# Kernel tuning notes

Measured on AMD Instinct MI355X. Metric: run time of the kernel, lower is better.

## Reference

```python
import jax, jax.numpy as jnp
from jax import lax
import numpy as np

B, W, V, E, H = 512, 40, 12000, 512, 512


def setup_inputs() -> dict:
    key = jax.random.key(0)
    ks = jax.random.split(key, 9)
    s = 0.05
    ques_vec = jax.random.randint(ks[0], (B, W), 0, V + 1)          # token ids, 0 = pad
    ques_len = jax.random.randint(ks[1], (B,), 1, W + 1)             # valid lengths in [1, W]
    lookup_W = jax.random.normal(ks[2], (E, V), jnp.float32) * s     # nn.Linear(vocab, emb).weight
    wih0 = jax.random.normal(ks[3], (2, 4 * H, E), jnp.float32) * s  # [dir, 4H, in]
    whh0 = jax.random.normal(ks[4], (2, 4 * H, H), jnp.float32) * s
    b0 = jax.random.normal(ks[5], (2, 2, 4 * H), jnp.float32) * s    # [dir, {b_ih,b_hh}, 4H]
    wih1 = jax.random.normal(ks[6], (2, 4 * H, 2 * H), jnp.float32) * s
    whh1 = jax.random.normal(ks[7], (2, 4 * H, H), jnp.float32) * s
    b1 = jax.random.normal(ks[8], (2, 2, 4 * H), jnp.float32) * s
    return {"ques_vec": ques_vec, "ques_len": ques_len, "lookup_W": lookup_W,
            "wih0": wih0, "whh0": whh0, "b0": b0,
            "wih1": wih1, "whh1": whh1, "b1": b1}


def _lstm_dir(x, wih, whh, b, reverse):
    # x: [B, T, D]; PyTorch gate order i, f, g, o
    Hc = whh.shape[1]
    xg = jnp.einsum('btd,gd->btg', x, wih) + b[0] + b[1]  # [B, T, 4H]
    xs = jnp.swapaxes(xg, 0, 1)                            # [T, B, 4H]
    if reverse:
        xs = xs[::-1]

    def step(carry, g_t):
        h, c = carry
        g = g_t + h @ whh.T
        i, f, gg, o = jnp.split(g, 4, axis=-1)
        c = jax.nn.sigmoid(f) * c + jax.nn.sigmoid(i) * jnp.tanh(gg)
        h = jax.nn.sigmoid(o) * jnp.tanh(c)
        return (h, c), h

    h0 = jnp.zeros((x.shape[0], Hc), x.dtype)
    _, hs = lax.scan(step, (h0, h0), xs)
    if reverse:
        hs = hs[::-1]
    return jnp.swapaxes(hs, 0, 1)  # [B, T, H]


def _bilstm(x, wih, whh, b):
    fwd = _lstm_dir(x, wih[0], whh[0], b[0], False)
    bwd = _lstm_dir(x, wih[1], whh[1], b[1], True)
    return jnp.concatenate([fwd, bwd], axis=-1)  # [B, T, 2H]


def reference(ques_vec, ques_len, lookup_W, wih0, whh0, b0, wih1, whh1, b1):
    # one-hot over vocab+1 with column 0 dropped == gather with id 0 -> zero vector
    table = jnp.concatenate([jnp.zeros((1, E), lookup_W.dtype), lookup_W.T], axis=0)  # [V+1, E]
    emb = jnp.tanh(table[ques_vec])          # [B, W, E] (dropout=0 -> identity)
    h = _bilstm(emb, wih0, whh0, b0)         # layer 0
    h = _bilstm(h, wih1, whh1, b1)           # layer 1 -> [B, W, 2H]
    # scatter-mask bmm == select hidden state at timestep ques_len-1
    idx = (ques_len - 1)[:, None, None]
    return jnp.take_along_axis(h, idx, axis=1).reshape(ques_vec.shape[0], -1)  # [B, 2H]
```

## Files before the change

### kernel.cpp

```cpp
#include <hip/hip_runtime.h>
#include <hip/hip_bf16.h>
#include <stdint.h>

#define NB 512
#define NW 40
#define NE 512
#define NH 512
#define NV 12000
#define G4 2048

typedef unsigned short u16;
typedef unsigned int u32;
typedef unsigned long long u64;
typedef __attribute__((ext_vector_type(8))) short short8;
typedef __attribute__((ext_vector_type(4))) float f32x4;

__device__ __forceinline__ unsigned short f2bf(float f) {
  unsigned int u = __float_as_uint(f);
  u += 0x7FFF + ((u >> 16) & 1);
  return (unsigned short)(u >> 16);
}
__device__ __forceinline__ float bf2f(unsigned short b) {
  return __uint_as_float(((unsigned int)b) << 16);
}
__device__ __forceinline__ float loadIn(const void* p, long i, int bf) {
  return bf ? bf2f(((const u16*)p)[i]) : ((const float*)p)[i];
}
__device__ __forceinline__ float fast_tanh(float x) {
  float ax = __builtin_fabsf(x);
  float t = 1.f - 2.f * __builtin_amdgcn_rcpf(__expf(ax + ax) + 1.f);
  return __builtin_copysignf(t, x);
}
__device__ __forceinline__ float sigm(float x) {
  return __builtin_amdgcn_rcpf(1.f + __expf(-x));
}

__global__ void detect_kernel(const u16* p, int* flag) {
  __shared__ int cnt;
  int i = threadIdx.x;
  if (i == 0) cnt = 0;
  __syncthreads();
  unsigned short u = p[2 * (i * 1001)];
  int e = (u >> 7) & 0xFF;
  if (e >= 100 && e <= 126) atomicAdd(&cnt, 1);
  __syncthreads();
  if (i == 0) *flag = (cnt >= 32) ? 1 : 0;
}

__global__ void table_kernel(const void* lookup, const int* flag, u16* tableT) {
  __shared__ float tile[64][65];
  int bf = *flag;
  int v0 = blockIdx.x * 64, e0 = blockIdx.y * 64;
  int tx = threadIdx.x, ty = threadIdx.y;
#pragma unroll
  for (int r = 0; r < 16; ++r) {
    int e = r * 4 + ty, v = tx;
    if (v0 + v < NV)
      tile[e][v] = tanhf(loadIn(lookup, (long)(e0 + e) * NV + v0 + v, bf));
  }
  __syncthreads();
#pragma unroll
  for (int r = 0; r < 16; ++r) {
    int v = r * 4 + ty, e = tx;
    if (v0 + v < NV)
      tableT[(long)(v0 + v) * NE + e0 + e] = f2bf(tile[e][v]);
  }
}

__global__ void embed_kernel(const int* __restrict__ qv,
                             const u16* __restrict__ tableT,
                             u16* __restrict__ emb) {
  int tid = blockIdx.x * 256 + threadIdx.x;
  int token = tid >> 6;
  int chunk = tid & 63;
  int tt = token / NB, b = token % NB;
  int q = qv[b * NW + tt];
  uint4 val = make_uint4(0u, 0u, 0u, 0u);
  if (q > 0) val = *(const uint4*)(tableT + (long)(q - 1) * NE + chunk * 8);
  *(uint4*)(emb + (long)token * NE + chunk * 8) = val;
}

__global__ void pack_kernel(const void* wih0, const void* whh0, const void* b0,
                            const void* wih1, const void* whh1, const void* b1,
                            const int* flag, u16* Wc0, u16* Wc1, float* bsum) {
  const long N0 = 2L * G4 * 1024, N1 = 2L * G4 * 1536;
  long idx = (long)blockIdx.x * 256 + threadIdx.x;
  int bf = *flag;
  if (idx < N0) {
    int d = (int)(idx / (G4 * 1024));
    int rem = (int)(idx % (long)(G4 * 1024));
    int g = rem / 1024, k = rem % 1024;
    float v = (k < 512) ? loadIn(wih0, ((long)d * G4 + g) * 512 + k, bf)
                        : loadIn(whh0, ((long)d * G4 + g) * 512 + (k - 512), bf);
    Wc0[idx] = f2bf(v);
  } else if (idx < N0 + N1) {
    long i2 = idx - N0;
    int d = (int)(i2 / (G4 * 1536));
    int rem = (int)(i2 % (long)(G4 * 1536));
    int g = rem / 1536, k = rem % 1536;
    float v = (k < 1024) ? loadIn(wih1, ((long)d * G4 + g) * 1024 + k, bf)
                         : loadIn(whh1, ((long)d * G4 + g) * 512 + (k - 1024), bf);
    Wc1[i2] = f2bf(v);
  } else if (idx < N0 + N1 + 2L * 2 * G4) {
    long i3 = idx - N0 - N1;
    int layer = (int)(i3 / (2 * G4));
    int d = (int)((i3 / G4) & 1);
    int g = (int)(i3 % G4);
    const void* bb = layer ? b1 : b0;
    float v = loadIn(bb, (long)d * 2 * G4 + g, bf) +
              loadIn(bb, (long)d * 2 * G4 + G4 + g, bf);
    bsum[i3] = v;
  }
}

__global__ void zero_bar(unsigned int* bar) {
  bar[blockIdx.x * 256 + threadIdx.x] = 0u;
}

__global__ __launch_bounds__(256, 2) void xg_gemm(
    const u16* __restrict__ X, int Kx, int Kfull, const u16* __restrict__ Wc,
    const float* __restrict__ bsumL, u16* __restrict__ xg) {
  __shared__ __align__(16) char lds[32768];
  const int tid = threadIdx.x;
  const int lane = tid & 63, wv = tid >> 6;
  const int wm = wv & 1, wn = wv >> 1;
  const int col = lane & 15, quad = lane >> 4;
  const int s = blockIdx.x >> 5, w = blockIdx.x & 31;
  const int bx = (s % 40) * 4 + (w & 3);
  const int by = (s / 40) * 8 + (w >> 2);
  const int tb0 = bx * 128;
  const int d = by >> 4, colb = by & 15, j0 = colb * 32;

  f32x4 zero = {0.f, 0.f, 0.f, 0.f};
  f32x4 acc[4][4];
#pragma unroll
  for (int i = 0; i < 4; ++i)
#pragma unroll
    for (int j = 0; j < 4; ++j) acc[i][j] = zero;

  const int iters = Kx >> 6;
  for (int it = 0; it < iters; ++it) {
    int k0 = it << 6;
#pragma unroll
    for (int p = 0; p < 8; ++p) {
      int c = p * 256 + tid;
      const u16* gsrc;
      if (c < 1024) {
        int r = c >> 3, sl = c & 7;
        int kk = k0 + ((sl * 8) ^ ((r & 7) << 3));
        gsrc = X + (long)(tb0 + r) * Kx + kk;
      } else {
        int cb = c - 1024;
        int r = cb >> 3, sl = cb & 7;
        int kk = k0 + ((sl * 8) ^ ((r & 7) << 3));
        int grow = (r >> 5) * 512 + j0 + (r & 31);
        gsrc = Wc + ((long)d * G4 + grow) * Kfull + kk;
      }
      __builtin_amdgcn_global_load_lds(
          (const __attribute__((address_space(1))) void*)(const void*)gsrc,
          (__attribute__((address_space(3))) void*)(lds + p * 4096 + wv * 1024),
          16, 0, 0);
    }
    __syncthreads();
    const u16* As = (const u16*)lds;
    const u16* Bs = (const u16*)(lds + 16384);
#pragma unroll
    for (int ks = 0; ks < 2; ++ks) {
      short8 afr[4], bfr[4];
#pragma unroll
      for (int mf = 0; mf < 4; ++mf) {
        int rm = wm * 64 + mf * 16 + col;
        int sl = (ks * 32 + quad * 8) ^ ((rm & 7) << 3);
        afr[mf] = *(const short8*)(As + rm * 64 + sl);
      }
#pragma unroll
      for (int nf = 0; nf < 4; ++nf) {
        int br = wn * 64 + nf * 16 + col;
        int sl = (ks * 32 + quad * 8) ^ ((br & 7) << 3);
        bfr[nf] = *(const short8*)(Bs + br * 64 + sl);
      }
#pragma unroll
      for (int mf = 0; mf < 4; ++mf)
#pragma unroll
        for (int nf = 0; nf < 4; ++nf)
          acc[mf][nf] = __builtin_amdgcn_mfma_f32_16x16x32_bf16(
              afr[mf], bfr[nf], acc[mf][nf], 0, 0, 0);
    }
    __syncthreads();
  }

  float bias[4];
#pragma unroll
  for (int nf = 0; nf < 4; ++nf) {
    int n = wn * 64 + nf * 16 + col;
    bias[nf] = bsumL[d * G4 + (n >> 5) * 512 + j0 + (n & 31)];
  }
#pragma unroll
  for (int mf = 0; mf < 4; ++mf)
#pragma unroll
    for (int nf = 0; nf < 4; ++nf) {
      int n = wn * 64 + nf * 16 + col;
      int g = n >> 5, jn = n & 31;
#pragma unroll
      for (int r = 0; r < 4; ++r) {
        int m = wm * 64 + mf * 16 + quad * 4 + r;
        int tb = tb0 + m, t = tb >> 9, b = tb & 511;
        long oi = ((((long)t * 2 + d) * 16 + colb) * 512 + b) * 128 + jn * 4 + g;
        xg[oi] = f2bf(acc[mf][nf][r] + bias[nf]);
      }
    }
}

__global__ __launch_bounds__(256, 1) void lstm_pers(
    const u16* __restrict__ xg, const u16* __restrict__ Wc, int Kfull, int Kx,
    u16* __restrict__ hbuf, u16* __restrict__ h0cat, void* __restrict__ outp,
    const int* __restrict__ qlen, const int* __restrict__ flag,
    unsigned int* bar, int layer) {
  __shared__ __align__(16) char lds[163840];
  const int tid = threadIdx.x;
  const int lane = tid & 63, wv = tid >> 6;
  const int col = lane & 15, quad = lane >> 4;
  const int l = blockIdx.x;
  const int colid = l & 31, mi = l >> 5;
  const int colb = colid & 15, d = colid >> 4;
  const int j0 = colb * 32;
  const int m0 = mi * 64;
  const int gid = l >> 4;
  const int r0 = wv * 16;

#pragma unroll
  for (int p = 0; p < 32; ++p) {
    int c = p * 256 + tid;
    int row = c >> 6, rem = c & 63;
    int kc = rem >> 3, sl = rem & 7;
    int grow = (row >> 5) * 512 + j0 + (row & 31);
    int gk = Kx + kc * 64 + ((sl * 8) ^ ((row & 7) << 3));
    const u16* gsrc = Wc + ((long)d * G4 + grow) * Kfull + gk;
    __builtin_amdgcn_global_load_lds(
        (const __attribute__((address_space(1))) void*)(const void*)gsrc,
        (__attribute__((address_space(3))) void*)(lds + p * 4096 + wv * 1024),
        16, 0, 0);
  }
  const u16* Bs = (const u16*)lds;
  char* wbuf = lds + 131072 + wv * 8192;
  u16* packb = (u16*)wbuf;

  float creg[2][4];
#pragma unroll
  for (int i = 0; i < 2; ++i)
#pragma unroll
    for (int r = 0; r < 4; ++r) creg[i][r] = 0.f;
  const int isbf = *flag;
  f32x4 zero = {0.f, 0.f, 0.f, 0.f};

  __syncthreads();

#pragma unroll 1
  for (int t = 0; t < NW; ++t) {
    const int tq = d ? (NW - 1 - t) : t;

    ushort4 xgv[2][4];
    const u16* xgt =
        xg + ((((long)tq * 2 + d) * 16 + colb) * 512 + m0 + r0) * 128;
#pragma unroll
    for (int js = 0; js < 2; ++js)
#pragma unroll
      for (int r = 0; r < 4; ++r)
        xgv[js][r] =
            *(const ushort4*)(xgt + (quad * 4 + r) * 128 + (js * 16 + col) * 4);
    __builtin_amdgcn_sched_barrier(0);

    f32x4 acc[8];
#pragma unroll
    for (int g = 0; g < 8; ++g) acc[g] = zero;

    if (t > 0) {
      {
        u32* sp = bar + ((gid * 4 + wv) << 4) + col;
        while (__ballot((int)(__hip_atomic_load(sp, __ATOMIC_RELAXED,
                                                __HIP_MEMORY_SCOPE_AGENT) <
                              (u32)t)))
          __builtin_amdgcn_s_sleep(1);
      }
      __builtin_amdgcn_sched_barrier(0);

      const u16* hp = hbuf + ((t - 1) & 1) * (2L * NB * NH) +
                      ((long)d * NB + m0 + r0) * NH;
      auto stage = [&](int it) {
        char* dst = wbuf + (it & 1) * 4096;
#pragma unroll
        for (int i = 0; i < 4; ++i) {
          int c = i * 64 + lane;
          int row = c >> 4, slot = c & 15;
          int half = slot >> 3, ck = slot & 7;
          int kk = it * 128 + half * 64 + ((ck * 8) ^ ((row & 7) << 3));
          const u16* gsrc = hp + (long)row * NH + kk;
          __builtin_amdgcn_global_load_lds(
              (const __attribute__((address_space(1))) void*)(const void*)gsrc,
              (__attribute__((address_space(3))) void*)(dst + i * 1024), 16, 0,
              16 );
        }
      };
      stage(0);
      stage(1);
#pragma unroll
      for (int it = 0; it < 4; ++it) {
        if (it < 3)
          asm volatile("s_waitcnt vmcnt(4)" ::: "memory");
        else
          asm volatile("s_waitcnt vmcnt(0)" ::: "memory");
        const u16* As = (const u16*)(wbuf + (it & 1) * 4096);
        short8 afr[4];
#pragma unroll
        for (int ks = 0; ks < 4; ++ks) {
          int ksub = ks * 32 + quad * 8;
          afr[ks] = *(const short8*)(As + col * 128 + (ksub & 64) +
                                     ((ksub & 63) ^ ((col & 7) << 3)));
        }
        if (it < 2) {
          asm volatile("s_waitcnt lgkmcnt(0)" ::: "memory");
          __builtin_amdgcn_sched_barrier(0);
          stage(it + 2);
        }
#pragma unroll
        for (int ks = 0; ks < 4; ++ks) {
          const int kc = it * 128 + ks * 32 + quad * 8;
#pragma unroll
          for (int nf = 0; nf < 8; ++nf) {
            int br = nf * 16 + col;
            int slb = (kc & 63) ^ ((br & 7) << 3);
            short8 bfr = *(const short8*)(Bs + br * 512 + (kc & ~63) + slb);
            acc[nf] = __builtin_amdgcn_mfma_f32_16x16x32_bf16(afr[ks], bfr,
                                                              acc[nf], 0, 0, 0);
          }
        }
      }
    }

#pragma unroll
    for (int js = 0; js < 2; ++js)
#pragma unroll
      for (int r = 0; r < 4; ++r) {
        const u16* xv = (const u16*)&xgv[js][r];
        float gi = acc[0 * 2 + js][r] + bf2f(xv[0]);
        float gf = acc[1 * 2 + js][r] + bf2f(xv[1]);
        float gg = acc[2 * 2 + js][r] + bf2f(xv[2]);
        float go = acc[3 * 2 + js][r] + bf2f(xv[3]);
        float si = sigm(gi);
        float sf = sigm(gf);
        float so = sigm(go);
        float cn = sf * creg[js][r] + si * fast_tanh(gg);
        float h = so * fast_tanh(cn);
        creg[js][r] = cn;
        packb[(quad * 4 + r) * 32 + js * 16 + col] = f2bf(h);
        if (layer == 1 && !isbf) {
          int bg = m0 + r0 + quad * 4 + r;
          if (qlen[bg] - 1 == tq)
            ((float*)outp)[(long)bg * (2 * NH) + d * NH + j0 + js * 16 + col] =
                h;
        }
      }

    const int srow = lane >> 2, part = lane & 3;
    u64 v0, v1;
    {
      const u64* pp = (const u64*)(packb + srow * 32 + part * 8);
      v0 = pp[0];
      v1 = pp[1];
    }
    u16* hnxt = hbuf + (t & 1) * (2L * NB * NH);
    {
      u64* hdst = (u64*)(hnxt + ((long)d * NB + m0 + r0 + srow) * NH + j0 +
                         part * 8);
      __hip_atomic_store(hdst, v0, __ATOMIC_RELAXED, __HIP_MEMORY_SCOPE_AGENT);
      __hip_atomic_store(hdst + 1, v1, __ATOMIC_RELAXED,
                         __HIP_MEMORY_SCOPE_AGENT);
    }

    if (t < NW - 1) {
      asm volatile("s_waitcnt vmcnt(0)" ::: "memory");
      if (lane == 0)
        __hip_atomic_store(bar + ((gid * 4 + wv) << 4) + colb, (u32)(t + 1),
                           __ATOMIC_RELAXED, __HIP_MEMORY_SCOPE_AGENT);
    }

    if (layer == 0) {
      u16* dst = h0cat + ((long)tq * NB + m0 + r0 + srow) * (2 * NH) + d * NH +
                 j0 + part * 8;
      *(u64*)dst = v0;
      *((u64*)dst + 1) = v1;
    } else if (isbf) {
      int bg = m0 + r0 + srow;
      if (qlen[bg] - 1 == tq) {
        u16* dst = (u16*)outp + (long)bg * (2 * NH) + d * NH + j0 + part * 8;
        *(u64*)dst = v0;
        *((u64*)dst + 1) = v1;
      }
    }
    __builtin_amdgcn_sched_barrier(0);
  }
}

extern "C" void kernel_launch(void* const* d_in, const int* in_sizes, int n_in,
                              void* d_out, int out_size, void* d_ws,
                              size_t ws_size, hipStream_t stream) {
  const int* qv = (const int*)d_in[0];
  const int* ql = (const int*)d_in[1];
  const void* lookup = d_in[2];
  const void* wih0 = d_in[3];
  const void* whh0 = d_in[4];
  const void* b0 = d_in[5];
  const void* wih1 = d_in[6];
  const void* whh1 = d_in[7];
  const void* b1 = d_in[8];

  char* ws = (char*)d_ws;
  size_t off = 0;
  int* flag = (int*)ws;                 off += 256;
  unsigned int* bar = (unsigned int*)(ws + off); off += 8192;
  float* bsum = (float*)(ws + off);     off += 2L * 2 * G4 * 4;
  u16* Wc0 = (u16*)(ws + off);          off += 2L * G4 * 1024 * 2;
  u16* Wc1 = (u16*)(ws + off);          off += 2L * G4 * 1536 * 2;
  u16* hbuf = (u16*)(ws + off);         off += 2L * 2 * NB * NH * 2;
  u16* h0cat = (u16*)(ws + off);        off += (size_t)NW * NB * 2 * NH * 2;
  u16* emb = (u16*)(ws + off);          off += (size_t)NW * NB * NE * 2;
  u16* xg = (u16*)(ws + off);           off += (size_t)NW * 2 * 16 * 512 * 128 * 2;
  u16* tableT = h0cat;

  detect_kernel<<<1, 64, 0, stream>>>((const u16*)lookup, flag);
  table_kernel<<<dim3(188, 8), dim3(64, 4), 0, stream>>>(lookup, flag, tableT);
  {
    long total = 2L * G4 * 1024 + 2L * G4 * 1536 + 2L * 2 * G4;
    int blocks = (int)((total + 255) / 256);
    pack_kernel<<<blocks, 256, 0, stream>>>(wih0, whh0, b0, wih1, whh1, b1,
                                            flag, Wc0, Wc1, bsum);
  }
  embed_kernel<<<NW * NB / 4, 256, 0, stream>>>(qv, tableT, emb);

  xg_gemm<<<5120, 256, 0, stream>>>(emb, 512, 1024, Wc0, bsum, xg);
  zero_bar<<<8, 256, 0, stream>>>(bar);
  lstm_pers<<<256, 256, 0, stream>>>(xg, Wc0, 1024, 512, hbuf, h0cat, d_out,
                                     ql, flag, bar, 0);
  xg_gemm<<<5120, 256, 0, stream>>>(h0cat, 1024, 1536, Wc1, bsum + 2 * G4, xg);
  zero_bar<<<8, 256, 0, stream>>>(bar);
  lstm_pers<<<256, 256, 0, stream>>>(xg, Wc1, 1536, 1024, hbuf, h0cat, d_out,
                                     ql, flag, bar, 1);
}
```

Measured before the change: 1.002 ms.

## Split persistent LSTM across 512 blocks with half-width column tiles

The persistent recurrent kernel now uses 512 blocks, each owning 16 hidden columns instead of 32. This halves the per-block LDS footprint so two blocks can be resident per CU, and spreads the serial per-timestep h@Whh work across more CUs. The layer-0 hidden output is written in a column-tiled layout, and the layer-1 input GEMM reads that layout through a new xtiled flag. The cost is more barrier flags to poll per step and smaller, less efficient MFMA tiles per wave.

```diff
diff --git a/kernel.cpp b/kernel.cpp
--- a/kernel.cpp
+++ b/kernel.cpp
@@ -118,8 +118,9 @@
 }
 
 __global__ __launch_bounds__(256, 2) void xg_gemm(
-    const u16* __restrict__ X, int Kx, int Kfull, const u16* __restrict__ Wc,
-    const float* __restrict__ bsumL, u16* __restrict__ xg) {
+    const u16* __restrict__ X, int Kx, int Kfull, int xtiled,
+    const u16* __restrict__ Wc, const float* __restrict__ bsumL,
+    u16* __restrict__ xg) {
   __shared__ __align__(16) char lds[32768];
   const int tid = threadIdx.x;
   const int lane = tid & 63, wv = tid >> 6;
@@ -148,7 +149,13 @@
       if (c < 1024) {
         int r = c >> 3, sl = c & 7;
         int kk = k0 + ((sl * 8) ^ ((r & 7) << 3));
-        gsrc = X + (long)(tb0 + r) * Kx + kk;
+        int tb = tb0 + r;
+        if (xtiled) {
+          gsrc = X + ((long)(tb >> 9) * 64 + (kk >> 4)) * 8192 +
+                 (long)(tb & 511) * 16 + (kk & 15);
+        } else {
+          gsrc = X + (long)tb * Kx + kk;
+        }
       } else {
         int cb = c - 1024;
         int r = cb >> 3, sl = cb & 7;
@@ -211,29 +218,29 @@
     }
 }
 
-__global__ __launch_bounds__(256, 1) void lstm_pers(
+__global__ __launch_bounds__(256, 2) void lstm_pers(
     const u16* __restrict__ xg, const u16* __restrict__ Wc, int Kfull, int Kx,
     u16* __restrict__ hbuf, u16* __restrict__ h0cat, void* __restrict__ outp,
     const int* __restrict__ qlen, const int* __restrict__ flag,
     unsigned int* bar, int layer) {
-  __shared__ __align__(16) char lds[163840];
+  __shared__ __align__(16) char lds[81920];
   const int tid = threadIdx.x;
   const int lane = tid & 63, wv = tid >> 6;
   const int col = lane & 15, quad = lane >> 4;
   const int l = blockIdx.x;
-  const int colid = l & 31, mi = l >> 5;
-  const int colb = colid & 15, d = colid >> 4;
-  const int j0 = colb * 32;
+  const int cb = l & 31;
+  const int gid = l >> 5;
+  const int d = gid & 1, mi = gid >> 1;
+  const int j0 = cb * 16;
   const int m0 = mi * 64;
-  const int gid = l >> 4;
   const int r0 = wv * 16;
 
 #pragma unroll
-  for (int p = 0; p < 32; ++p) {
+  for (int p = 0; p < 16; ++p) {
     int c = p * 256 + tid;
     int row = c >> 6, rem = c & 63;
     int kc = rem >> 3, sl = rem & 7;
-    int grow = (row >> 5) * 512 + j0 + (row & 31);
+    int grow = (row >> 4) * 512 + j0 + (row & 15);
     int gk = Kx + kc * 64 + ((sl * 8) ^ ((row & 7) << 3));
     const u16* gsrc = Wc + ((long)d * G4 + grow) * Kfull + gk;
     __builtin_amdgcn_global_load_lds(
@@ -242,14 +249,12 @@
         16, 0, 0);
   }
   const u16* Bs = (const u16*)lds;
-  char* wbuf = lds + 131072 + wv * 8192;
+  char* wbuf = lds + 65536 + wv * 4096;
   u16* packb = (u16*)wbuf;
 
-  float creg[2][4];
-#pragma unroll
-  for (int i = 0; i < 2; ++i)
-#pragma unroll
-    for (int r = 0; r < 4; ++r) creg[i][r] = 0.f;
+  float creg[4];
+#pragma unroll
+  for (int r = 0; r < 4; ++r) creg[r] = 0.f;
   const int isbf = *flag;
   f32x4 zero = {0.f, 0.f, 0.f, 0.f};
 
@@ -259,24 +264,22 @@
   for (int t = 0; t < NW; ++t) {
     const int tq = d ? (NW - 1 - t) : t;
 
-    ushort4 xgv[2][4];
+    ushort4 xgv[4];
     const u16* xgt =
-        xg + ((((long)tq * 2 + d) * 16 + colb) * 512 + m0 + r0) * 128;
-#pragma unroll
-    for (int js = 0; js < 2; ++js)
-#pragma unroll
-      for (int r = 0; r < 4; ++r)
-        xgv[js][r] =
-            *(const ushort4*)(xgt + (quad * 4 + r) * 128 + (js * 16 + col) * 4);
+        xg + ((((long)tq * 2 + d) * 16 + (cb >> 1)) * 512 + m0 + r0) * 128;
+#pragma unroll
+    for (int r = 0; r < 4; ++r)
+      xgv[r] =
+          *(const ushort4*)(xgt + (quad * 4 + r) * 128 + ((cb & 1) * 16 + col) * 4);
     __builtin_amdgcn_sched_barrier(0);
 
-    f32x4 acc[8];
-#pragma unroll
-    for (int g = 0; g < 8; ++g) acc[g] = zero;
+    f32x4 acc[4];
+#pragma unroll
+    for (int g = 0; g < 4; ++g) acc[g] = zero;
 
     if (t > 0) {
       {
-        u32* sp = bar + ((gid * 4 + wv) << 4) + col;
+        u32* sp = bar + ((gid * 4 + wv) << 5) + (lane & 31);
         while (__ballot((int)(__hip_atomic_load(sp, __ATOMIC_RELAXED,
                                                 __HIP_MEMORY_SCOPE_AGENT) <
                               (u32)t)))
@@ -287,13 +290,12 @@
       const u16* hp = hbuf + ((t - 1) & 1) * (2L * NB * NH) +
                       ((long)d * NB + m0 + r0) * NH;
       auto stage = [&](int it) {
-        char* dst = wbuf + (it & 1) * 4096;
-#pragma unroll
-        for (int i = 0; i < 4; ++i) {
+        char* dst = wbuf + (it & 1) * 2048;
+#pragma unroll
+        for (int i = 0; i < 2; ++i) {
           int c = i * 64 + lane;
-          int row = c >> 4, slot = c & 15;
-          int half = slot >> 3, ck = slot & 7;
-          int kk = it * 128 + half * 64 + ((ck * 8) ^ ((row & 7) << 3));
+          int row = c >> 3, slot = c & 7;
+          int kk = it * 64 + ((slot * 8) ^ ((row & 7) << 3));
           const u16* gsrc = hp + (long)row * NH + kk;
           __builtin_amdgcn_global_load_lds(
               (const __attribute__((address_space(1))) void*)(const void*)gsrc,
@@ -303,30 +305,29 @@
       };
       stage(0);
       stage(1);
-#pragma unroll
-      for (int it = 0; it < 4; ++it) {
-        if (it < 3)
-          asm volatile("s_waitcnt vmcnt(4)" ::: "memory");
+#pragma unroll 1
+      for (int it = 0; it < 8; ++it) {
+        if (it < 7)
+          asm volatile("s_waitcnt vmcnt(2)" ::: "memory");
         else
           asm volatile("s_waitcnt vmcnt(0)" ::: "memory");
-        const u16* As = (const u16*)(wbuf + (it & 1) * 4096);
-        short8 afr[4];
-#pragma unroll
-        for (int ks = 0; ks < 4; ++ks) {
+        const u16* As = (const u16*)(wbuf + (it & 1) * 2048);
+        short8 afr[2];
+#pragma unroll
+        for (int ks = 0; ks < 2; ++ks) {
           int ksub = ks * 32 + quad * 8;
-          afr[ks] = *(const short8*)(As + col * 128 + (ksub & 64) +
-                                     ((ksub & 63) ^ ((col & 7) << 3)));
+          afr[ks] = *(const short8*)(As + col * 64 + (ksub ^ ((col & 7) << 3)));
         }
-        if (it < 2) {
+        if (it < 6) {
           asm volatile("s_waitcnt lgkmcnt(0)" ::: "memory");
           __builtin_amdgcn_sched_barrier(0);
           stage(it + 2);
         }
 #pragma unroll
-        for (int ks = 0; ks < 4; ++ks) {
-          const int kc = it * 128 + ks * 32 + quad * 8;
-#pragma unroll
-          for (int nf = 0; nf < 8; ++nf) {
+        for (int ks = 0; ks < 2; ++ks) {
+          const int kc = it * 64 + ks * 32 + quad * 8;
+#pragma unroll
+          for (int nf = 0; nf < 4; ++nf) {
             int br = nf * 16 + col;
             int slb = (kc & 63) ^ ((br & 7) << 3);
             short8 bfr = *(const short8*)(Bs + br * 512 + (kc & ~63) + slb);
@@ -338,63 +339,49 @@
     }
 
 #pragma unroll
-    for (int js = 0; js < 2; ++js)
-#pragma unroll
-      for (int r = 0; r < 4; ++r) {
-        const u16* xv = (const u16*)&xgv[js][r];
-        float gi = acc[0 * 2 + js][r] + bf2f(xv[0]);
-        float gf = acc[1 * 2 + js][r] + bf2f(xv[1]);
-        float gg = acc[2 * 2 + js][r] + bf2f(xv[2]);
-        float go = acc[3 * 2 + js][r] + bf2f(xv[3]);
-        float si = sigm(gi);
-        float sf = sigm(gf);
-        float so = sigm(go);
-        float cn = sf * creg[js][r] + si * fast_tanh(gg);
-        float h = so * fast_tanh(cn);
-        creg[js][r] = cn;
-        packb[(quad * 4 + r) * 32 + js * 16 + col] = f2bf(h);
-        if (layer == 1 && !isbf) {
-          int bg = m0 + r0 + quad * 4 + r;
-          if (qlen[bg] - 1 == tq)
-            ((float*)outp)[(long)bg * (2 * NH) + d * NH + j0 + js * 16 + col] =
-                h;
-        }
-      }
+    for (int r = 0; r < 4; ++r) {
+      const u16* xv = (const u16*)&xgv[r];
+      float gi = acc[0][r] + bf2f(xv[0]);
+      float gf = acc[1][r] + bf2f(xv[1]);
+      float gg = acc[2][r] + bf2f(xv[2]);
+      float go = acc[3][r] + bf2f(xv[3]);
+      float si = sigm(gi);
+      float sf = sigm(gf);
+      float so = sigm(go);
+      float cn = sf * creg[r] + si * fast_tanh(gg);
+      float h = so * fast_tanh(cn);
+      creg[r] = cn;
+      packb[(quad * 4 + r) * 16 + col] = f2bf(h);
+      if (layer == 1 && !isbf) {
+        int bg = m0 + r0 + quad * 4 + r;
+        if (qlen[bg] - 1 == tq)
+          ((float*)outp)[(long)bg * (2 * NH) + d * NH + j0 + col] = h;
+      }
+    }
 
     const int srow = lane >> 2, part = lane & 3;
-    u64 v0, v1;
-    {
-      const u64* pp = (const u64*)(packb + srow * 32 + part * 8);
-      v0 = pp[0];
-      v1 = pp[1];
-    }
+    u64 v0 = *(const u64*)(packb + srow * 16 + part * 4);
     u16* hnxt = hbuf + (t & 1) * (2L * NB * NH);
-    {
-      u64* hdst = (u64*)(hnxt + ((long)d * NB + m0 + r0 + srow) * NH + j0 +
-                         part * 8);
-      __hip_atomic_store(hdst, v0, __ATOMIC_RELAXED, __HIP_MEMORY_SCOPE_AGENT);
-      __hip_atomic_store(hdst + 1, v1, __ATOMIC_RELAXED,
-                         __HIP_MEMORY_SCOPE_AGENT);
-    }
+    __hip_atomic_store(
+        (u64*)(hnxt + ((long)d * NB + m0 + r0 + srow) * NH + j0 + part * 4), v0,
+        __ATOMIC_RELAXED, __HIP_MEMORY_SCOPE_AGENT);
 
     if (t < NW - 1) {
       asm volatile("s_waitcnt vmcnt(0)" ::: "memory");
       if (lane == 0)
-        __hip_atomic_store(bar + ((gid * 4 + wv) << 4) + colb, (u32)(t + 1),
+        __hip_atomic_store(bar + ((gid * 4 + wv) << 5) + cb, (u32)(t + 1),
                            __ATOMIC_RELAXED, __HIP_MEMORY_SCOPE_AGENT);
     }
 
     if (layer == 0) {
-      u16* dst = h0cat + ((long)tq * NB + m0 + r0 + srow) * (2 * NH) + d * NH +
-                 j0 + part * 8;
+      u16* dst = h0cat + ((((long)tq * 2 + d) * 32 + cb) * 512 +
+                          (m0 + r0 + srow)) * 16 + part * 4;
       *(u64*)dst = v0;
-      *((u64*)dst + 1) = v1;
     } else if (isbf) {
       int bg = m0 + r0 + srow;
       if (qlen[bg] - 1 == tq) {
-        u16* dst = (u16*)outp + (long)bg * (2 * NH) + d * NH + j0 + part * 8;
+        u16* dst = (u16*)outp + (long)bg * (2 * NH) + d * NH + j0 + part * 4;
         *(u64*)dst = v0;
-        *((u64*)dst + 1) = v1;
       }
     }
     __builtin_amdgcn_sched_barrier(0);
@@ -437,12 +424,13 @@
   }
   embed_kernel<<<NW * NB / 4, 256, 0, stream>>>(qv, tableT, emb);
 
-  xg_gemm<<<5120, 256, 0, stream>>>(emb, 512, 1024, Wc0, bsum, xg);
+  xg_gemm<<<5120, 256, 0, stream>>>(emb, 512, 1024, 0, Wc0, bsum, xg);
   zero_bar<<<8, 256, 0, stream>>>(bar);
-  lstm_pers<<<256, 256, 0, stream>>>(xg, Wc0, 1024, 512, hbuf, h0cat, d_out,
+  lstm_pers<<<512, 256, 0, stream>>>(xg, Wc0, 1024, 512, hbuf, h0cat, d_out,
                                      ql, flag, bar, 0);
-  xg_gemm<<<5120, 256, 0, stream>>>(h0cat, 1024, 1536, Wc1, bsum + 2 * G4, xg);
+  xg_gemm<<<5120, 256, 0, stream>>>(h0cat, 1024, 1536, 1, Wc1, bsum + 2 * G4,
+                                    xg);
   zero_bar<<<8, 256, 0, stream>>>(bar);
-  lstm_pers<<<256, 256, 0, stream>>>(xg, Wc1, 1536, 1024, hbuf, h0cat, d_out,
+  lstm_pers<<<512, 256, 0, stream>>>(xg, Wc1, 1536, 1024, hbuf, h0cat, d_out,
                                      ql, flag, bar, 1);
 }
```

New measurement: 1.144 ms. +14.1%, slower.
